# Performance work log

Measured on AMD Instinct MI355X. Metric: run time of the kernel, lower is better.

## Reference

```python
import jax, jax.numpy as jnp
import numpy as np

B, D, N, WD, R, NW = 1024, 1024, 256, 64, 4, 1
EPS = 1e-6


def _dense(x, W, b):
    return x @ W + b


def _cosine_weights(memory, keys, strengths):
    # memory [B,N,WD], keys [B,K,WD], strengths [B,K] -> softmax cosine weights [B,K,N]
    dot = jnp.einsum('bkw,bnw->bkn', keys, memory)
    mn = jnp.linalg.norm(memory, axis=-1)  # [B,N]
    kn = jnp.linalg.norm(keys, axis=-1)    # [B,K]
    sim = dot / (kn[:, :, None] * mn[:, None, :] + EPS)
    return jax.nn.softmax(sim * strengths[:, :, None], axis=-1)


def _allocation(usage):
    # DNC Freeness allocation: sort by non-usage, exclusive cumprod of usage, unsort.
    usage = EPS + (1.0 - EPS) * usage
    nonusage = 1.0 - usage
    idx = jnp.argsort(-nonusage, axis=-1)            # descending non-usage
    s_non = jnp.take_along_axis(nonusage, idx, axis=-1)
    s_use = 1.0 - s_non
    cp = jnp.cumprod(s_use, axis=-1)
    excl = jnp.concatenate([jnp.ones_like(cp[:, :1]), cp[:, :-1]], axis=-1)
    s_alloc = s_non * excl
    inv = jnp.argsort(idx, axis=-1)                  # inverse permutation
    return jnp.take_along_axis(s_alloc, inv, axis=-1)


def _forward(controller, memory, prev_read_weights, prev_write_weights, prev_link,
             prev_precedence, prev_usage, params):
    (W_wv, b_wv, W_ev, b_ev, W_fg, b_fg, W_ag, b_ag, W_wg, b_wg,
     W_rm, b_rm, W_ws, b_ws, W_rs, b_rs, W_wk, b_wk, W_rk, b_rk) = params
    Bsz = controller.shape[0]

    # _read_inputs: small dense projections of controller output
    write_vectors = _dense(controller, W_wv, b_wv).reshape(Bsz, NW, WD)
    erase_vectors = jax.nn.sigmoid(_dense(controller, W_ev, b_ev)).reshape(Bsz, NW, WD)
    free_gate = jax.nn.sigmoid(_dense(controller, W_fg, b_fg))          # [B,R]
    allocation_gate = jax.nn.sigmoid(_dense(controller, W_ag, b_ag))    # [B,NW]
    write_gate = jax.nn.sigmoid(_dense(controller, W_wg, b_wg))         # [B,NW]
    read_mode = jax.nn.softmax(_dense(controller, W_rm, b_rm).reshape(Bsz, R, 1 + 2 * NW), axis=-1)
    write_keys = _dense(controller, W_wk, b_wk).reshape(Bsz, NW, WD)
    write_strengths = jax.nn.softplus(_dense(controller, W_ws, b_ws))   # [B,NW]
    read_keys = _dense(controller, W_rk, b_rk).reshape(Bsz, R, WD)
    read_strengths = jax.nn.softplus(_dense(controller, W_rs, b_rs))    # [B,R]

    # Freeness: usage update (not differentiable wrt write weights, per DNC)
    ww_sg = jax.lax.stop_gradient(prev_write_weights)
    agg_ww = 1.0 - jnp.prod(1.0 - ww_sg, axis=1)                        # [B,N]
    usage_after_write = prev_usage + (1.0 - prev_usage) * agg_ww
    phi = jnp.prod(1.0 - free_gate[:, :, None] * prev_read_weights, axis=1)
    usage = usage_after_write * phi

    # write weights: content + allocation mixed by gates
    write_content = _cosine_weights(memory, write_keys, write_strengths)  # [B,NW,N]
    write_gates = allocation_gate * write_gate
    alloc_list = []
    u = usage
    for i in range(NW):
        a = _allocation(u)
        alloc_list.append(a)
        u = u + (1.0 - u) * write_gates[:, i:i + 1] * a
    write_alloc = jnp.stack(alloc_list, axis=1)                           # [B,NW,N]
    ag = allocation_gate[:, :, None]
    wg = write_gate[:, :, None]
    write_weights = wg * (ag * write_alloc + (1.0 - ag) * write_content)

    # erase and write
    weighted_resets = write_weights[:, :, :, None] * erase_vectors[:, :, None, :]  # [B,NW,N,WD]
    reset_gate = jnp.prod(1.0 - weighted_resets, axis=1)                           # [B,N,WD]
    memory = memory * reset_gate + jnp.einsum('bwn,bwd->bnd', write_weights, write_vectors)

    # temporal linkage update
    ww_i = write_weights[:, :, :, None]
    ww_j = write_weights[:, :, None, :]
    new_link = ww_i * prev_precedence[:, :, None, :]
    link = (1.0 - ww_i - ww_j) * prev_link + new_link
    link = link * (1.0 - jnp.eye(N, dtype=link.dtype))                   # zero diagonal
    precedence = (1.0 - jnp.sum(write_weights, axis=-1, keepdims=True)) * prev_precedence + write_weights

    # read weights: content + directional (forward/backward over link)
    read_content = _cosine_weights(memory, read_keys, read_strengths)    # [B,R,N]
    forward_w = jnp.einsum('brn,bwmn->brwm', prev_read_weights, link)    # adjoint_b=True
    backward_w = jnp.einsum('brn,bwnm->brwm', prev_read_weights, link)
    backward_mode = read_mode[:, :, :NW]
    forward_mode = read_mode[:, :, NW:2 * NW]
    content_mode = read_mode[:, :, 2 * NW]
    read_weights = (content_mode[:, :, None] * read_content
                    + jnp.einsum('brw,brwn->brn', forward_mode, forward_w)
                    + jnp.einsum('brw,brwn->brn', backward_mode, backward_w))
    read_words = jnp.einsum('brn,bnd->brd', read_weights, memory)        # [B,R,WD]
    return read_words, memory, read_weights, write_weights, link, precedence, usage


def setup_inputs() -> dict:
    key = jax.random.key(0)
    ks = jax.random.split(key, 32)
    inp = {
        'controller': jax.random.normal(ks[0], (B, D), jnp.float32),
        'memory': jax.random.normal(ks[1], (B, N, WD), jnp.float32),
        'prev_read_weights': jax.random.uniform(ks[2], (B, R, N), jnp.float32) / N,
        'prev_write_weights': jax.random.uniform(ks[3], (B, NW, N), jnp.float32) / N,
        'prev_link': jnp.zeros((B, NW, N, N), jnp.float32),
        'prev_precedence': jax.random.uniform(ks[4], (B, NW, N), jnp.float32) / N,
        'prev_usage': jax.random.uniform(ks[5], (B, N), jnp.float32),
    }
    dims = [('wv', NW * WD), ('ev', NW * WD), ('fg', R), ('ag', NW), ('wg', NW),
            ('rm', R * (1 + 2 * NW)), ('ws', NW), ('rs', R), ('wk', NW * WD), ('rk', R * WD)]
    i = 6
    for name, od in dims:
        inp['W_' + name] = jax.random.normal(ks[i], (D, od), jnp.float32) * 0.02
        inp['b_' + name] = jnp.zeros((od,), jnp.float32)
        i += 1
    return inp


def reference(controller, memory, prev_read_weights, prev_write_weights, prev_link,
              prev_precedence, prev_usage,
              W_wv, b_wv, W_ev, b_ev, W_fg, b_fg, W_ag, b_ag, W_wg, b_wg,
              W_rm, b_rm, W_ws, b_ws, W_rs, b_rs, W_wk, b_wk, W_rk, b_rk):
    params = (W_wv, b_wv, W_ev, b_ev, W_fg, b_fg, W_ag, b_ag, W_wg, b_wg,
              W_rm, b_rm, W_ws, b_ws, W_rs, b_rs, W_wk, b_wk, W_rk, b_rk)
    return _forward(controller, memory, prev_read_weights, prev_write_weights,
                    prev_link, prev_precedence, prev_usage, params)
```

## Files before the change

kernel.cpp:

```cpp
#include <hip/hip_runtime.h>
#include <math.h>

typedef unsigned short ush;
typedef float v4f __attribute__((ext_vector_type(4)));

#define EPSc 1e-6f

#define NB 1024
#define ND 1024
#define NN 256
#define NWD 64
#define NR 4

#define OFF_RWORDS   ((size_t)0)
#define OFF_MEM      ((size_t)262144)
#define OFF_RWEIGHTS ((size_t)17039360)
#define OFF_WW       ((size_t)18087936)
#define OFF_LINK     ((size_t)18350080)
#define OFF_PREC     ((size_t)85458944)
#define OFF_USAGE    ((size_t)85721088)

#define WS_PART   ((size_t)0)
#define WS_PARAMS ((size_t)2097152)
#define WS_FW     ((size_t)2785280)

struct Ptrs {
  const float* W[10];
  const float* Bv[10];
};

__device__ __forceinline__ float b2f(ush h){
  union { unsigned int u; float f; } v; v.u = ((unsigned int)h) << 16; return v.f;
}
__device__ __forceinline__ ush f2b(float f){
  union { float f; unsigned int u; } v; v.f = f;
  unsigned int u = v.u;
  u += 0x7fffu + ((u >> 16) & 1u);
  return (ush)(u >> 16);
}
__device__ __forceinline__ float sigm(float x){ return 1.f/(1.f+expf(-x)); }
__device__ __forceinline__ float softplus(float x){ return fmaxf(x,0.f) + log1pf(expf(-fabsf(x))); }

__device__ __forceinline__ int colmap(int c, int& lc, int& od){
  const int starts[11] = {0,64,128,132,133,134,146,147,151,215,471};
  const int ods[10]    = {64,64,4,1,1,12,1,4,64,256};
  int m = 0;
  #pragma unroll
  for (int i=1;i<10;i++) if (c >= starts[i]) m = i;
  lc = c - starts[m]; od = ods[m];
  return m;
}

__global__ __launch_bounds__(512) void k1_gemm(const float* __restrict__ ctrl, Ptrs P,
                                               float* __restrict__ part){
  int bt = blockIdx.x;
  int kc = blockIdx.y;
  int t  = threadIdx.x;
  __shared__ float cl[8*260];
  {
    int row = t >> 6, chunk = t & 63;
    const float* src = ctrl + (size_t)(bt*8+row)*ND + kc*256 + chunk*4;
    *(float4*)&cl[row*260 + chunk*4] = *(const float4*)src;
  }
  __syncthreads();
  int c = (t < 471) ? t : 470;
  int lc, od; int m = colmap(c, lc, od);
  const float* wp = P.W[m];
  float acc[8];
  #pragma unroll
  for (int r=0;r<8;r++) acc[r]=0.f;
  #pragma unroll 4
  for (int d = 0; d < 256; d++){
    int dg = kc*256 + d;
    float wv = wp[(size_t)dg*od + lc];
    #pragma unroll
    for (int r = 0; r < 8; r++)
      acc[r] += cl[r*260 + d]*wv;
  }
  if (t < 471){
    #pragma unroll
    for (int r=0;r<8;r++)
      part[((size_t)kc*NB + bt*8+r)*512 + c] = acc[r];
  }
}


#define SSTAGE(j,k) { \
  float kp = __shfl_xor(key, (j)); int ip = __shfl_xor(idx, (j)); \
  bool gt = (key > kp) || (key == kp && idx > ip); \
  bool selmin = (((t & (k)) == 0) == ((t & (j)) == 0)); \
  if (selmin == gt){ key = kp; idx = ip; } }

#define LSTAGE(j,k) { \
  sk[t] = key; si[t] = idx; __syncthreads(); \
  float kp = sk[t^(j)]; int ip = si[t^(j)]; \
  bool gt = (key > kp) || (key == kp && idx > ip); \
  bool selmin = (((t & (k)) == 0) == ((t & (j)) == 0)); \
  if (selmin == gt){ key = kp; idx = ip; } \
  __syncthreads(); }

__global__ __launch_bounds__(256) void k2_gates(
    const float* __restrict__ part, Ptrs P,
    const float* __restrict__ mem, const float* __restrict__ prw_in,
    const float* __restrict__ pww_in, const float* __restrict__ pprec,
    const float* __restrict__ pusage,
    float* __restrict__ params,
    float* __restrict__ out_ww, float* __restrict__ out_prec, float* __restrict__ out_usage)
{
  int b = blockIdx.x, t = threadIdx.x;
  int w = t >> 6, l = t & 63;
  __shared__ float proj[512];
  __shared__ float wkL[64];
  __shared__ float scal[12];
  __shared__ float wred[16];
  __shared__ float sk[256];
  __shared__ int   si[256];
  __shared__ float salloc[256];

  for (int c = t; c < 471; c += 256){
    float v = 0.f;
    #pragma unroll
    for (int kc=0;kc<4;kc++) v += part[((size_t)kc*NB + b)*512 + c];
    int lc, od; int m = colmap(c, lc, od);
    v += P.Bv[m][lc];
    proj[c] = v;
  }
  __syncthreads();

  float* pb = params + (size_t)b*672;
  if (t < 64){
    pb[t] = proj[t];
    pb[64+t] = sigm(proj[64+t]);
    wkL[t] = proj[151+t];
  }
  pb[128 + t] = proj[215 + t];
  if (t < 4){
    pb[384 + t] = softplus(proj[147 + t]);
    float a = proj[134 + 3*t], bq = proj[134 + 3*t + 1], c2 = proj[134 + 3*t + 2];
    float mx = fmaxf(a, fmaxf(bq, c2));
    float ea = expf(a-mx), eb = expf(bq-mx), ec = expf(c2-mx);
    float s = ea+eb+ec;
    pb[388 + 3*t]     = ea/s;
    pb[388 + 3*t + 1] = eb/s;
    pb[388 + 3*t + 2] = ec/s;
    scal[t] = sigm(proj[128+t]);
  }
  if (t == 0){
    scal[4] = sigm(proj[132]);
    scal[5] = sigm(proj[133]);
    scal[6] = softplus(proj[146]);
  }
  if (w == 0){
    float kv = proj[151 + l];
    float s2 = kv*kv;
    #pragma unroll
    for (int off=32; off>0; off>>=1) s2 += __shfl_xor(s2, off);
    if (l == 0) scal[7] = sqrtf(s2);
  }
  __syncthreads();

  float us;
  {
    float pu = pusage[(size_t)b*NN + t];
    float pw = pww_in[(size_t)b*NN + t];
    float uaw = pu + (1.f-pu)*pw;
    float phi = 1.f;
    #pragma unroll
    for (int r=0;r<4;r++)
      phi *= (1.f - scal[r]*prw_in[((size_t)b*NR + r)*NN + t]);
    us = uaw*phi;
    out_usage[(size_t)b*NN + t] = us;
  }

  float sim;
  {
    const float* mrow = mem + ((size_t)b*NN + t)*NWD;
    float dot = 0.f, n2 = 0.f;
    for (int d0=0; d0<64; d0+=4){
      float4 q = *(const float4*)(mrow + d0);
      dot += wkL[d0]*q.x + wkL[d0+1]*q.y + wkL[d0+2]*q.z + wkL[d0+3]*q.w;
      n2  += q.x*q.x + q.y*q.y + q.z*q.z + q.w*q.w;
    }
    sim = scal[6]*dot/(scal[7]*sqrtf(n2) + EPSc);
  }
  {
    float m_ = sim;
    #pragma unroll
    for (int off=32; off>0; off>>=1) m_ = fmaxf(m_, __shfl_xor(m_, off));
    if (l == 0) wred[w] = m_;
  }
  __syncthreads();
  float mx = fmaxf(fmaxf(wred[0],wred[1]), fmaxf(wred[2],wred[3]));
  float e = expf(sim - mx);
  {
    float s_ = e;
    #pragma unroll
    for (int off=32; off>0; off>>=1) s_ += __shfl_xor(s_, off);
    if (l == 0) wred[4+w] = s_;
  }
  __syncthreads();
  float content = e / (wred[4]+wred[5]+wred[6]+wred[7]);

  float key = EPSc + (1.f-EPSc)*us;
  int idx = t;
  SSTAGE(1,2)
  SSTAGE(2,4)  SSTAGE(1,4)
  SSTAGE(4,8)  SSTAGE(2,8)  SSTAGE(1,8)
  SSTAGE(8,16) SSTAGE(4,16) SSTAGE(2,16) SSTAGE(1,16)
  SSTAGE(16,32) SSTAGE(8,32) SSTAGE(4,32) SSTAGE(2,32) SSTAGE(1,32)
  SSTAGE(32,64) SSTAGE(16,64) SSTAGE(8,64) SSTAGE(4,64) SSTAGE(2,64) SSTAGE(1,64)
  LSTAGE(64,128)
  SSTAGE(32,128) SSTAGE(16,128) SSTAGE(8,128) SSTAGE(4,128) SSTAGE(2,128) SSTAGE(1,128)
  LSTAGE(128,256)
  LSTAGE(64,256)
  SSTAGE(32,256) SSTAGE(16,256) SSTAGE(8,256) SSTAGE(4,256) SSTAGE(2,256) SSTAGE(1,256)

  float v = key;
  #pragma unroll
  for (int off=1; off<64; off<<=1){
    float u = __shfl_up(v, off);
    if (l >= off) v *= u;
  }
  if (l == 63) wred[8+w] = v;
  __syncthreads();
  float pre = 1.f;
  #pragma unroll
  for (int q=0; q<3; q++) if (q < w) pre *= wred[8+q];
  float exv = __shfl_up(v, 1);
  if (l == 0) exv = 1.f;
  float excl = exv * pre;
  float s_alloc = (1.f - key) * excl;
  salloc[idx] = s_alloc;
  __syncthreads();
  float alloc = salloc[t];

  float ag = scal[4], wg = scal[5];
  float ww = wg*(ag*alloc + (1.f-ag)*content);
  pb[400 + t] = ww;
  out_ww[(size_t)b*NN + t] = ww;
  {
    float s_ = ww;
    #pragma unroll
    for (int off=32; off>0; off>>=1) s_ += __shfl_xor(s_, off);
    if (l == 0) wred[12+w] = s_;
  }
  __syncthreads();
  float wsum = wred[12]+wred[13]+wred[14]+wred[15];
  float prec = (1.f - wsum)*pprec[(size_t)b*NN + t] + ww;
  out_prec[(size_t)b*NN + t] = prec;
}

__global__ __launch_bounds__(256) void k4_link(
    const float* __restrict__ plink, const float* __restrict__ pprec,
    const float* __restrict__ prw_in, const float* __restrict__ params,
    float* __restrict__ out_link, float* __restrict__ fw, float* __restrict__ bwp)
{
  int b = blockIdx.x, cc = blockIdx.y, t = threadIdx.x;
  int w = t >> 6, l = t & 63;
  __shared__ float wwl[256], ppl[256], prwl[4*256];
  __shared__ v4f   bred[4][4][64];
  __shared__ float fwbuf[4*128];
  const float* pb = params + (size_t)b*672;
  wwl[t] = pb[400 + t];
  ppl[t] = pprec[(size_t)b*NN + t];
  #pragma unroll
  for (int r=0;r<4;r++) prwl[r*256 + t] = prw_in[((size_t)b*NR + r)*NN + t];
  __syncthreads();

  v4f wwj = *(const v4f*)&wwl[4*l];
  v4f ppj = *(const v4f*)&ppl[4*l];
  v4f pr0 = *(const v4f*)&prwl[0*256 + 4*l];
  v4f pr1 = *(const v4f*)&prwl[1*256 + 4*l];
  v4f pr2 = *(const v4f*)&prwl[2*256 + 4*l];
  v4f pr3 = *(const v4f*)&prwl[3*256 + 4*l];

  v4f bacc0 = {0.f,0.f,0.f,0.f}, bacc1 = bacc0, bacc2 = bacc0, bacc3 = bacc0;

  int i0 = cc*128 + w*32;
  const v4f* plrow = (const v4f*)(plink + ((size_t)b*NN + i0)*NN) + l;
  float*     olbase = out_link + ((size_t)b*NN + i0)*NN + 4*l;

  for (int k=0; k<32; k++){
    int i = i0 + k;
    v4f pl = plrow[(size_t)k*64];
    float wwi = wwl[i];
    float c1  = 1.f - wwi;
    float pi0 = prwl[0*256+i], pi1 = prwl[1*256+i],
          pi2 = prwl[2*256+i], pi3 = prwl[3*256+i];
    v4f lv = (c1 - wwj)*pl + wwi*ppj;
    if (l == (i>>2)) lv[i&3] = 0.f;
    __builtin_nontemporal_store(lv, (v4f*)(olbase + (size_t)k*NN));

    v4f f0 = pr0*lv, f1 = pr1*lv, f2 = pr2*lv, f3 = pr3*lv;
    float s0 = f0.x+f0.y+f0.z+f0.w;
    float s1 = f1.x+f1.y+f1.z+f1.w;
    float s2 = f2.x+f2.y+f2.z+f2.w;
    float s3 = f3.x+f3.y+f3.z+f3.w;
    bacc0 += pi0*lv; bacc1 += pi1*lv; bacc2 += pi2*lv; bacc3 += pi3*lv;

    s0 += __shfl_xor(s0,1); s0 += __shfl_xor(s0,2);
    s1 += __shfl_xor(s1,1); s1 += __shfl_xor(s1,2);
    s2 += __shfl_xor(s2,1); s2 += __shfl_xor(s2,2);
    s3 += __shfl_xor(s3,1); s3 += __shfl_xor(s3,2);
    float v = (l&1) ? ((l&2)? s3 : s1) : ((l&2)? s2 : s0);
    v += __shfl_xor(v,4); v += __shfl_xor(v,8);
    v += __shfl_xor(v,16); v += __shfl_xor(v,32);
    if (l < 4) fwbuf[w*128 + l*32 + k] = v;
  }

  bred[w][0][l] = bacc0;
  bred[w][1][l] = bacc1;
  bred[w][2][l] = bacc2;
  bred[w][3][l] = bacc3;
  __syncthreads();

  {
    int r = t >> 6, l2 = t & 63;
    v4f a = bred[0][r][l2], b4 = bred[1][r][l2],
        c4 = bred[2][r][l2], d4 = bred[3][r][l2];
    v4f s = a + b4 + c4 + d4;
    *(v4f*)&bwp[(((size_t)cc*NB + b)*NR + r)*NN + 4*l2] = s;
    #pragma unroll
    for (int e=0;e<2;e++){
      int idx = t + e*256;
      int rr = idx >> 7, j = idx & 127;
      fw[((size_t)b*NR + rr)*NN + cc*128 + j] = fwbuf[(j>>5)*128 + rr*32 + (j&31)];
    }
  }
}

__global__ __launch_bounds__(256) void k5_read(
    const float* __restrict__ mem, const float* __restrict__ params,
    const float* __restrict__ fw, const float* __restrict__ bwp,
    float* __restrict__ out_rwords, float* __restrict__ out_mem, float* __restrict__ out_rweights)
{
  int b = blockIdx.x, t = threadIdx.x;
  __shared__ ush   memn[256*66];
  __shared__ float wvl[64], erl[64], rkl[256];
  __shared__ float siml[4*260];
  __shared__ float rwl[4*260];
  __shared__ float scal[32];
  const float* pb = params + (size_t)b*672;
  if (t < 64){ wvl[t] = pb[t]; erl[t] = pb[64+t]; }
  rkl[t] = pb[128 + t];
  if (t < 4)  scal[12+t] = pb[384+t];
  if (t < 12) scal[16+t] = pb[388+t];
  __syncthreads();
  if (t < 4){
    float s = 0.f;
    for (int d=0;d<64;d++){ float v = rkl[t*64+d]; s += v*v; }
    scal[t] = sqrtf(s);
  }
  __syncthreads();

  float wwn = pb[400 + t];
  const float* mrow = mem + ((size_t)b*NN + t)*NWD;
  float* orow = out_mem + ((size_t)b*NN + t)*NWD;
  float n2=0.f, dot0=0.f, dot1=0.f, dot2=0.f, dot3=0.f;
  for (int d0=0; d0<64; d0+=4){
    float4 q = *(const float4*)(mrow + d0);
    float4 qo;
    float* qi = (float*)&q;
    float* po = (float*)&qo;
    #pragma unroll
    for (int k=0;k<4;k++){
      int d = d0+k;
      float m = qi[k];
      float nv = m*(1.f - wwn*erl[d]) + wwn*wvl[d];
      po[k] = nv;
      n2 += nv*nv;
      dot0 += rkl[0*64+d]*nv;
      dot1 += rkl[1*64+d]*nv;
      dot2 += rkl[2*64+d]*nv;
      dot3 += rkl[3*64+d]*nv;
    }
    unsigned int p01 = (unsigned int)f2b(po[0]) | ((unsigned int)f2b(po[1]) << 16);
    unsigned int p23 = (unsigned int)f2b(po[2]) | ((unsigned int)f2b(po[3]) << 16);
    *(unsigned int*)&memn[t*66 + d0]     = p01;
    *(unsigned int*)&memn[t*66 + d0 + 2] = p23;
    *(float4*)(orow + d0) = qo;
  }
  float sn = sqrtf(n2);
  siml[0*260+t] = scal[12]*dot0/(scal[0]*sn + EPSc);
  siml[1*260+t] = scal[13]*dot1/(scal[1]*sn + EPSc);
  siml[2*260+t] = scal[14]*dot2/(scal[2]*sn + EPSc);
  siml[3*260+t] = scal[15]*dot3/(scal[3]*sn + EPSc);
  __syncthreads();

  int rr = t >> 6, lane = t & 63;
  {
    float m1 = -1e30f;
    #pragma unroll
    for (int q2=0;q2<4;q2++) m1 = fmaxf(m1, siml[rr*260 + q2*64 + lane]);
    #pragma unroll
    for (int off=32; off>0; off>>=1) m1 = fmaxf(m1, __shfl_xor(m1, off));
    float s1 = 0.f;
    #pragma unroll
    for (int q2=0;q2<4;q2++) s1 += expf(siml[rr*260 + q2*64 + lane] - m1);
    #pragma unroll
    for (int off=32; off>0; off>>=1) s1 += __shfl_xor(s1, off);
    if (lane == 0){ scal[4+rr] = m1; scal[8+rr] = s1; }
  }
  __syncthreads();

  #pragma unroll
  for (int r=0;r<4;r++){
    float c = expf(siml[r*260+t] - scal[4+r]) / scal[8+r];
    float fwv = fw[((size_t)b*NR + r)*NN + t];
    float bwv = bwp[((size_t)b*NR + r)*NN + t]
              + bwp[((size_t)(NB + b)*NR + r)*NN + t];
    float rwv = scal[16+3*r+2]*c + scal[16+3*r+1]*fwv + scal[16+3*r+0]*bwv;
    rwl[r*260 + t] = rwv;
    out_rweights[((size_t)b*NR + r)*NN + t] = rwv;
  }
  __syncthreads();

  {
    float acc = 0.f;
    for (int n=0;n<256;n++) acc += rwl[rr*260 + n]*b2f(memn[n*66 + lane]);
    out_rwords[((size_t)b*NR + rr)*NWD + lane] = acc;
  }
}

extern "C" void kernel_launch(void* const* d_in, const int* in_sizes, int n_in,
                              void* d_out, int out_size, void* d_ws, size_t ws_size,
                              hipStream_t stream) {
  const float* ctrl   = (const float*)d_in[0];
  const float* mem    = (const float*)d_in[1];
  const float* prw    = (const float*)d_in[2];
  const float* pww    = (const float*)d_in[3];
  const float* plink  = (const float*)d_in[4];
  const float* pprec  = (const float*)d_in[5];
  const float* pusage = (const float*)d_in[6];
  Ptrs P;
  for (int i=0;i<10;i++){
    P.W[i]  = (const float*)d_in[7 + 2*i];
    P.Bv[i] = (const float*)d_in[8 + 2*i];
  }
  float* ws = (float*)d_ws;
  float* part   = ws + WS_PART;
  float* params = ws + WS_PARAMS;
  float* fw     = ws + WS_FW;

  float* o = (float*)d_out;
  float* out_rwords   = o + OFF_RWORDS;
  float* out_mem      = o + OFF_MEM;
  float* out_rweights = o + OFF_RWEIGHTS;
  float* out_ww       = o + OFF_WW;
  float* out_link     = o + OFF_LINK;
  float* out_prec     = o + OFF_PREC;
  float* out_usage    = o + OFF_USAGE;

  k1_gemm<<<dim3(128,4), 512, 0, stream>>>(ctrl, P, part);
  k2_gates<<<NB, 256, 0, stream>>>(part, P, mem, prw, pww, pprec, pusage,
                                   params, out_ww, out_prec, out_usage);
  k4_link<<<dim3(NB,2), 256, 0, stream>>>(plink, pprec, prw, params, out_link, fw, part);
  k5_read<<<NB, 256, 0, stream>>>(mem, params, fw, part,
                                  out_rwords, out_mem, out_rweights);
}
```

Baseline: 735.3 us.

## Rework projection GEMM, unroll link loop, transpose bf16 memory tile in read kernel

The projection GEMM now runs 256 threads that each compute two output columns. It reads controller rows straight from global memory as float4 instead of staging them in shared memory, which removes the barrier and raises per-thread work. The link update loop gets a modest unroll. The read kernel stores the updated memory in shared memory transposed, as bf16 with word-dimension-major layout, so the final read-word reduction can use 128-bit vector loads of eight bf16 values. The trade-offs are more registers and more redundant global loads in the GEMM, plus scalar 16-bit shared stores with a possible bank-conflict change on the write side.

```diff
diff --git a/kernel.cpp b/kernel.cpp
--- a/kernel.cpp
+++ b/kernel.cpp
@@ -38,6 +38,12 @@
   u += 0x7fffu + ((u >> 16) & 1u);
   return (ush)(u >> 16);
 }
+__device__ __forceinline__ float u16lo(unsigned int w){
+  union { unsigned int u; float f; } v; v.u = w << 16; return v.f;
+}
+__device__ __forceinline__ float u16hi(unsigned int w){
+  union { unsigned int u; float f; } v; v.u = w & 0xffff0000u; return v.f;
+}
 __device__ __forceinline__ float sigm(float x){ return 1.f/(1.f+expf(-x)); }
 __device__ __forceinline__ float softplus(float x){ return fmaxf(x,0.f) + log1pf(expf(-fabsf(x))); }
 
@@ -51,36 +57,47 @@
   return m;
 }
 
-__global__ __launch_bounds__(512) void k1_gemm(const float* __restrict__ ctrl, Ptrs P,
+__global__ __launch_bounds__(256) void k1_gemm(const float* __restrict__ ctrl, Ptrs P,
                                                float* __restrict__ part){
   int bt = blockIdx.x;
   int kc = blockIdx.y;
   int t  = threadIdx.x;
-  __shared__ float cl[8*260];
-  {
-    int row = t >> 6, chunk = t & 63;
-    const float* src = ctrl + (size_t)(bt*8+row)*ND + kc*256 + chunk*4;
-    *(float4*)&cl[row*260 + chunk*4] = *(const float4*)src;
-  }
-  __syncthreads();
-  int c = (t < 471) ? t : 470;
-  int lc, od; int m = colmap(c, lc, od);
-  const float* wp = P.W[m];
-  float acc[8];
-  #pragma unroll
-  for (int r=0;r<8;r++) acc[r]=0.f;
-  #pragma unroll 4
-  for (int d = 0; d < 256; d++){
-    int dg = kc*256 + d;
-    float wv = wp[(size_t)dg*od + lc];
-    #pragma unroll
-    for (int r = 0; r < 8; r++)
-      acc[r] += cl[r*260 + d]*wv;
-  }
-  if (t < 471){
+  int c0 = t;
+  bool has1 = (t + 256 < 471);
+  int c1 = has1 ? t + 256 : 470;
+  int lc0, od0, lc1, od1;
+  int m0 = colmap(c0, lc0, od0);
+  int m1 = colmap(c1, lc1, od1);
+  const float* w0p = P.W[m0] + lc0;
+  const float* w1p = P.W[m1] + lc1;
+  float acc0[8], acc1[8];
+  #pragma unroll
+  for (int r=0;r<8;r++){ acc0[r]=0.f; acc1[r]=0.f; }
+  const float* cb = ctrl + (size_t)(bt*8)*ND + kc*256;
+  for (int d0 = 0; d0 < 256; d0 += 4){
+    float4 cv[8];
+    #pragma unroll
+    for (int r=0;r<8;r++) cv[r] = *(const float4*)(cb + (size_t)r*ND + d0);
+    #pragma unroll
+    for (int k=0;k<4;k++){
+      size_t dg = (size_t)(kc*256 + d0 + k);
+      float wv0 = w0p[dg*od0];
+      float wv1 = w1p[dg*od1];
+      #pragma unroll
+      for (int r=0;r<8;r++){
+        float cvk = ((const float*)&cv[r])[k];
+        acc0[r] += cvk*wv0;
+        acc1[r] += cvk*wv1;
+      }
+    }
+  }
+  #pragma unroll
+  for (int r=0;r<8;r++)
+    part[((size_t)kc*NB + bt*8+r)*512 + c0] = acc0[r];
+  if (has1){
     #pragma unroll
     for (int r=0;r<8;r++)
-      part[((size_t)kc*NB + bt*8+r)*512 + c] = acc[r];
+      part[((size_t)kc*NB + bt*8+r)*512 + c1] = acc1[r];
   }
 }
 
@@ -280,6 +297,7 @@
   const v4f* plrow = (const v4f*)(plink + ((size_t)b*NN + i0)*NN) + l;
   float*     olbase = out_link + ((size_t)b*NN + i0)*NN + 4*l;
 
+  #pragma unroll 2
   for (int k=0; k<32; k++){
     int i = i0 + k;
     v4f pl = plrow[(size_t)k*64];
@@ -329,13 +347,14 @@
   }
 }
 
+#define MSTR 264
 __global__ __launch_bounds__(256) void k5_read(
     const float* __restrict__ mem, const float* __restrict__ params,
     const float* __restrict__ fw, const float* __restrict__ bwp,
     float* __restrict__ out_rwords, float* __restrict__ out_mem, float* __restrict__ out_rweights)
 {
   int b = blockIdx.x, t = threadIdx.x;
-  __shared__ ush   memn[256*66];
+  __shared__ ush   memt[64*MSTR];
   __shared__ float wvl[64], erl[64], rkl[256];
   __shared__ float siml[4*260];
   __shared__ float rwl[4*260];
@@ -373,11 +392,8 @@
       dot1 += rkl[1*64+d]*nv;
       dot2 += rkl[2*64+d]*nv;
       dot3 += rkl[3*64+d]*nv;
+      memt[d*MSTR + t] = f2b(nv);
     }
-    unsigned int p01 = (unsigned int)f2b(po[0]) | ((unsigned int)f2b(po[1]) << 16);
-    unsigned int p23 = (unsigned int)f2b(po[2]) | ((unsigned int)f2b(po[3]) << 16);
-    *(unsigned int*)&memn[t*66 + d0]     = p01;
-    *(unsigned int*)&memn[t*66 + d0 + 2] = p23;
     *(float4*)(orow + d0) = qo;
   }
   float sn = sqrtf(n2);
@@ -417,7 +433,18 @@
 
   {
     float acc = 0.f;
-    for (int n=0;n<256;n++) acc += rwl[rr*260 + n]*b2f(memn[n*66 + lane]);
+    const ush* mcol = &memt[lane*MSTR];
+    const float* rrow = &rwl[rr*260];
+    #pragma unroll 4
+    for (int q=0; q<32; q++){
+      uint4  u  = *(const uint4*)(mcol + 8*q);
+      float4 ra = *(const float4*)(rrow + 8*q);
+      float4 rb = *(const float4*)(rrow + 8*q + 4);
+      acc += ra.x*u16lo(u.x) + ra.y*u16hi(u.x)
+           + ra.z*u16lo(u.y) + ra.w*u16hi(u.y)
+           + rb.x*u16lo(u.z) + rb.y*u16hi(u.z)
+           + rb.z*u16lo(u.w) + rb.w*u16hi(u.w);
+    }
     out_rwords[((size_t)b*NR + rr)*NWD + lane] = acc;
   }
 }
@@ -451,7 +478,7 @@
   float* out_prec     = o + OFF_PREC;
   float* out_usage    = o + OFF_USAGE;
 
-  k1_gemm<<<dim3(128,4), 512, 0, stream>>>(ctrl, P, part);
+  k1_gemm<<<dim3(128,4), 256, 0, stream>>>(ctrl, P, part);
   k2_gates<<<NB, 256, 0, stream>>>(part, P, mem, prw, pww, pprec, pusage,
                                    params, out_ww, out_prec, out_usage);
   k4_link<<<dim3(NB,2), 256, 0, stream>>>(plink, pprec, prw, params, out_link, fw, part);
```

Measured after the change: 778.2 us. 1.06x slower.
